# Kernel optimization log

Measured on AMD Instinct MI355X. Metric: run time of the kernel, lower is better.

Reference implementation:

```python
import jax, jax.numpy as jnp
import numpy as np

B, T, D, H, K = 2, 2048, 1024, 16, 4
DH = D // H  # 64 head dim
EPS_L2 = 1e-6
EPS_RMS = 1e-6


def setup_inputs() -> dict:
    key = jax.random.key(0)
    ks = jax.random.split(key, 10)
    s = 0.02
    return {
        'x': jax.random.normal(ks[0], (B, T, D), jnp.float32),
        'Wq': jax.random.normal(ks[1], (D, D), jnp.float32) * s,
        'Wk': jax.random.normal(ks[2], (D, D), jnp.float32) * s,
        'Wv': jax.random.normal(ks[3], (D, D), jnp.float32) * s,
        'Wb': jax.random.normal(ks[4], (D, H), jnp.float32) * s,
        'conv_q': jax.random.normal(ks[5], (D, K), jnp.float32) * 0.5,
        'conv_k': jax.random.normal(ks[6], (D, K), jnp.float32) * 0.5,
        'conv_v': jax.random.normal(ks[7], (D, K), jnp.float32) * 0.5,
        'rms_g': jnp.ones((DH,), jnp.float32),
        'Wo': jax.random.normal(ks[8], (D, D), jnp.float32) * s,
    }


def _silu(u):
    return u * jax.nn.sigmoid(u)


def _short_conv(x, w):
    # causal depthwise conv1d, x: [B,T,C], w: [C,K]; y[t] = sum_i w[:,i]*x[t-(K-1)+i]
    k = w.shape[1]
    xp = jnp.pad(x, ((0, 0), (k - 1, 0), (0, 0)))
    y = xp[:, 0:T, :] * w[:, 0]
    for i in range(1, k):
        y = y + xp[:, i:i + T, :] * w[:, i]
    return y


def _l2norm(u):
    return u * jax.lax.rsqrt(jnp.sum(u * u, axis=-1, keepdims=True) + EPS_L2)


def reference(x, Wq, Wk, Wv, Wb, conv_q, conv_k, conv_v, rms_g, Wo):
    # projections + causal short conv (silu fused, as in fla ShortConvolution)
    q = _silu(_short_conv(x @ Wq, conv_q)).reshape(B, T, H, DH)
    k = _silu(_short_conv(x @ Wk, conv_k)).reshape(B, T, H, DH)
    v = _silu(_short_conv(x @ Wv, conv_v)).reshape(B, T, H, DH)
    q = _l2norm(q)
    k = _l2norm(k)
    beta = jax.nn.sigmoid(x @ Wb)  # [B,T,H]

    # time-major for scan
    qs = q.transpose(1, 0, 2, 3)  # [T,B,H,DH]
    ks_ = k.transpose(1, 0, 2, 3)
    vs = v.transpose(1, 0, 2, 3)
    bs = beta.transpose(1, 0, 2)  # [T,B,H]

    def step(S, inp):
        # S: [B,H,dk,dv]; delta rule: S <- S + beta * k (v - k^T S)^T
        q_t, k_t, v_t, b_t = inp
        kS = jnp.einsum('bhk,bhkv->bhv', k_t, S)
        S = S + jnp.einsum('bhk,bhv->bhkv', k_t, b_t[..., None] * (v_t - kS))
        o_t = jnp.einsum('bhk,bhkv->bhv', q_t, S)
        return S, o_t

    S0 = jnp.zeros((B, H, DH, DH), x.dtype)
    _, o = jax.lax.scan(step, S0, (qs, ks_, vs, bs))  # o: [T,B,H,DH]
    o = o.transpose(1, 0, 2, 3)  # [B,T,H,DH]

    # per-head RMSNorm then output projection
    o = o * jax.lax.rsqrt(jnp.mean(o * o, axis=-1, keepdims=True) + EPS_RMS) * rms_g
    return o.reshape(B, T, D) @ Wo
```

## Files before the change

kernel.cpp:

```cpp
#include <hip/hip_runtime.h>
#include <hip/hip_bf16.h>
#include <math.h>

#define B_ 2
#define T_ 2048
#define D_ 1024
#define H_ 16
#define DH_ 64
#define M_ (B_*T_)
#define NC_ 32
#define CS_ 64
#define NCH_ (B_*H_*NC_)
#define QKVN_ 3072

typedef __attribute__((ext_vector_type(4))) float floatx4;
typedef __attribute__((ext_vector_type(8))) short short8;

__device__ __forceinline__ ushort f2bf(float f) {
  union { float f; unsigned u; } c; c.f = f;
  unsigned r = (c.u + 0x7FFFu + ((c.u >> 16) & 1u)) >> 16;
  return (ushort)r;
}
__device__ __forceinline__ float siluf(float u) {
  return u / (1.f + __expf(-u));
}
__device__ __forceinline__ float f4get(const float4& v, int j) {
  return j == 0 ? v.x : j == 1 ? v.y : j == 2 ? v.z : v.w;
}
__device__ __forceinline__ float rdlane(float v, int l) {
  return __int_as_float(__builtin_amdgcn_readlane(__float_as_int(v), l));
}
__device__ __forceinline__ int ksw(int r, int c) { return ((c ^ (r >> 4)) << 2); }

__global__ void cast_kernel(const float* __restrict__ in, ushort* __restrict__ out, int n4) {
  int i = blockIdx.x * blockDim.x + threadIdx.x;
  if (i >= n4) return;
  float4 v = ((const float4*)in)[i];
  ushort4 o;
  o.x = f2bf(v.x); o.y = f2bf(v.y); o.z = f2bf(v.z); o.w = f2bf(v.w);
  ((ushort4*)out)[i] = o;
}

__global__ void transpose_cast_kernel(const float* __restrict__ W, ushort* __restrict__ Wt,
                                      int K, int N) {
  __shared__ float tile[32][33];
  int tx = threadIdx.x, ty = threadIdx.y;
  int n0 = blockIdx.x * 32, k0 = blockIdx.y * 32;
  #pragma unroll
  for (int i = 0; i < 32; i += 8)
    tile[ty + i][tx] = W[(size_t)(k0 + ty + i) * N + n0 + tx];
  __syncthreads();
  #pragma unroll
  for (int i = 0; i < 32; i += 8)
    Wt[(size_t)(n0 + ty + i) * K + k0 + tx] = f2bf(tile[tx][ty + i]);
}

__global__ void transpose_wb_kernel(const float* __restrict__ Wb, float* __restrict__ WbT) {
  int bk = blockIdx.x;
  int tid = threadIdx.x;
  int kl = tid >> 4, h = tid & 15;
  int k = bk * 16 + kl;
  WbT[(size_t)h * D_ + k] = Wb[(size_t)k * H_ + h];
}

__global__ __launch_bounds__(256) void gemm128_kernel(
    const ushort* __restrict__ A, const ushort* __restrict__ Bt,
    float* __restrict__ C, int M, int N, int K) {
  __shared__ ushort lA[128 * 32];
  __shared__ ushort lB[128 * 32];
  int tid = threadIdx.x;
  int wave = tid >> 6, lane = tid & 63;
  int wm = wave >> 1, wn = wave & 1;
  int m16 = lane & 15, q4 = lane >> 4;
  int bm = blockIdx.x, bn = blockIdx.y;
  floatx4 acc[4][4] = {};
  int srow = tid >> 2;
  int sk8 = tid & 3;
  const ushort* Ag = A + (size_t)(bm * 128 + srow) * K + sk8 * 8;
  const ushort* Bg = Bt + (size_t)(bn * 128 + srow) * K + sk8 * 8;
  ushort* lAp = lA + tid * 8;
  ushort* lBp = lB + tid * 8;
  for (int k0 = 0; k0 < K; k0 += 32) {
    __builtin_amdgcn_global_load_lds(
        (const __attribute__((address_space(1))) void*)(Ag + k0),
        (__attribute__((address_space(3))) void*)lAp, 16, 0, 0);
    __builtin_amdgcn_global_load_lds(
        (const __attribute__((address_space(1))) void*)(Ag + (size_t)64 * K + k0),
        (__attribute__((address_space(3))) void*)(lAp + 2048), 16, 0, 0);
    __builtin_amdgcn_global_load_lds(
        (const __attribute__((address_space(1))) void*)(Bg + k0),
        (__attribute__((address_space(3))) void*)lBp, 16, 0, 0);
    __builtin_amdgcn_global_load_lds(
        (const __attribute__((address_space(1))) void*)(Bg + (size_t)64 * K + k0),
        (__attribute__((address_space(3))) void*)(lBp + 2048), 16, 0, 0);
    __syncthreads();
    short8 af[4], bf[4];
    #pragma unroll
    for (int i = 0; i < 4; i++) {
      af[i] = *(short8*)&lA[(wm * 64 + i * 16 + m16) * 32 + q4 * 8];
      bf[i] = *(short8*)&lB[(wn * 64 + i * 16 + m16) * 32 + q4 * 8];
    }
    #pragma unroll
    for (int mi = 0; mi < 4; mi++)
      #pragma unroll
      for (int nj = 0; nj < 4; nj++)
        acc[mi][nj] = __builtin_amdgcn_mfma_f32_16x16x32_bf16(af[mi], bf[nj], acc[mi][nj], 0, 0, 0);
    __syncthreads();
  }
  float* Cb = C + (size_t)(bm * 128) * N + bn * 128;
  #pragma unroll
  for (int mi = 0; mi < 4; mi++) {
    #pragma unroll
    for (int nj = 0; nj < 4; nj++) {
      #pragma unroll
      for (int i = 0; i < 4; i++) {
        int row = wm * 64 + mi * 16 + q4 * 4 + i;
        int col = wn * 64 + nj * 16 + m16;
        Cb[(size_t)row * N + col] = acc[mi][nj][i];
      }
    }
  }
}

__global__ __launch_bounds__(256) void beta_kernel(const float* __restrict__ x,
                                                   const float* __restrict__ WbT,
                                                   float* __restrict__ beta) {
  __shared__ __align__(16) float xs[D_];
  int row = blockIdx.x;
  int tid = threadIdx.x;
  ((float4*)xs)[tid] = ((const float4*)(x + (size_t)row * D_))[tid];
  __syncthreads();
  int h = tid >> 4;
  int seg = tid & 15;
  const float4* wrow = (const float4*)(WbT + (size_t)h * D_) + seg * 16;
  const float4* xsrow = (const float4*)xs + seg * 16;
  float s = 0.f;
  #pragma unroll
  for (int j = 0; j < 16; j++) {
    int jj = (j + seg) & 15;
    float4 xv = xsrow[jj];
    float4 wv = wrow[jj];
    s += xv.x * wv.x + xv.y * wv.y + xv.z * wv.z + xv.w * wv.w;
  }
  #pragma unroll
  for (int off = 8; off; off >>= 1) s += __shfl_down(s, off, 16);
  if (seg == 0) beta[(size_t)row * H_ + h] = 1.f / (1.f + __expf(-s));
}

__global__ __launch_bounds__(256) void conv_kernel(
    const float* __restrict__ qkv,
    const float* __restrict__ cq, const float* __restrict__ ck, const float* __restrict__ cv,
    float* __restrict__ qo, float* __restrict__ ko, float* __restrict__ vo) {
  int row = blockIdx.x;
  int t = row & (T_ - 1);
  int tid = threadIdx.x;
  int c0 = tid * 4;
  float4 zf = {0.f, 0.f, 0.f, 0.f};
  float4 xq[4], xk[4], xv[4];
  #pragma unroll
  for (int i = 0; i < 4; i++) {
    int tt = t - 3 + i;
    if (tt >= 0) {
      const float* rp = qkv + (size_t)(row - 3 + i) * QKVN_;
      xq[i] = *(const float4*)(rp + c0);
      xk[i] = *(const float4*)(rp + 1024 + c0);
      xv[i] = *(const float4*)(rp + 2048 + c0);
    } else { xq[i] = zf; xk[i] = zf; xv[i] = zf; }
  }
  float yq[4], yk[4], yv[4];
  float pq = 0.f, pk = 0.f;
  #pragma unroll
  for (int j = 0; j < 4; j++) {
    float4 wq = ((const float4*)cq)[c0 + j];
    float4 wk = ((const float4*)ck)[c0 + j];
    float4 wv = ((const float4*)cv)[c0 + j];
    float sq = 0.f, sk = 0.f, sv = 0.f;
    #pragma unroll
    for (int i = 0; i < 4; i++) {
      sq += f4get(wq, i) * f4get(xq[i], j);
      sk += f4get(wk, i) * f4get(xk[i], j);
      sv += f4get(wv, i) * f4get(xv[i], j);
    }
    yq[j] = siluf(sq); yk[j] = siluf(sk); yv[j] = siluf(sv);
    pq += yq[j] * yq[j]; pk += yk[j] * yk[j];
  }
  #pragma unroll
  for (int off = 1; off < 16; off <<= 1) {
    pq += __shfl_xor(pq, off, 16);
    pk += __shfl_xor(pk, off, 16);
  }
  float rq = rsqrtf(pq + 1e-6f), rk = rsqrtf(pk + 1e-6f);
  float4 oq = {yq[0]*rq, yq[1]*rq, yq[2]*rq, yq[3]*rq};
  float4 okk = {yk[0]*rk, yk[1]*rk, yk[2]*rk, yk[3]*rk};
  float4 ov = {yv[0], yv[1], yv[2], yv[3]};
  *(float4*)(qo + (size_t)row * D_ + c0) = oq;
  *(float4*)(ko + (size_t)row * D_ + c0) = okk;
  *(float4*)(vo + (size_t)row * D_ + c0) = ov;
}

__global__ __launch_bounds__(256) void prep1_kernel(
    const float* __restrict__ kn, const float* __restrict__ vn,
    const float* __restrict__ beta,
    float* __restrict__ Wkbuf, float* __restrict__ U0buf) {
  __shared__ __align__(16) float Ash[64 * 68];
  __shared__ float bsh[64];
  __shared__ __align__(16) float uni[5312];
  float (*Ksh)[68] = (float (*)[68])uni;
  float (*Tsh)[16][20] = (float (*)[16][20])uni;
  float (*Msh)[16][20] = (float (*)[16][20])(uni + 1280);
  float (*Xsh)[132] = (float (*)[132])(uni + 3200);

  int ch = blockIdx.x;
  int b = ch >> 9, h = (ch >> 5) & 15, c = ch & 31;
  int tid = threadIdx.x;
  int t = tid >> 2, seg = tid & 3;
  int wave = tid >> 6, lane = tid & 63;
  int r = lane >> 2, q = lane & 3;
  const float* krow = kn + ((size_t)(b * T_ + c * 64 + t)) * D_ + h * 64;
  #pragma unroll
  for (int g = 0; g < 4; g++)
    *(float4*)&Ksh[t][ksw(t, seg * 4 + g)] = *(const float4*)&krow[seg * 16 + 4 * g];
  if (tid < 64) bsh[tid] = beta[((size_t)(b * T_ + c * 64 + tid)) * H_ + h];
  __syncthreads();
  {
    int qt = tid >> 4, qs = tid & 15;
    int swt = qt >> 2, sws = qs >> 2;
    float acc[4][4];
    #pragma unroll
    for (int i = 0; i < 4; i++)
      #pragma unroll
      for (int j = 0; j < 4; j++) acc[i][j] = 0.f;
    for (int d4 = 0; d4 < 16; d4++) {
      float4 kt[4], ks[4];
      #pragma unroll
      for (int i = 0; i < 4; i++) kt[i] = *(float4*)&Ksh[qt * 4 + i][((d4 ^ swt) << 2)];
      #pragma unroll
      for (int j = 0; j < 4; j++) ks[j] = *(float4*)&Ksh[qs * 4 + j][((d4 ^ sws) << 2)];
      #pragma unroll
      for (int i = 0; i < 4; i++)
        #pragma unroll
        for (int j = 0; j < 4; j++)
          acc[i][j] += kt[i].x * ks[j].x + kt[i].y * ks[j].y
                     + kt[i].z * ks[j].z + kt[i].w * ks[j].w;
    }
    #pragma unroll
    for (int i = 0; i < 4; i++) {
      int row = qt * 4 + i;
      float bt = bsh[row];
      float4 a4;
      a4.x = (row > qs * 4 + 0) ? bt * acc[i][0] : 0.f;
      a4.y = (row > qs * 4 + 1) ? bt * acc[i][1] : 0.f;
      a4.z = (row > qs * 4 + 2) ? bt * acc[i][2] : 0.f;
      a4.w = (row > qs * 4 + 3) ? bt * acc[i][3] : 0.f;
      *(float4*)&Ash[row * 68 + qs * 4] = a4;
    }
  }
  float xk[16], xv[16];
  {
    float bt = bsh[t];
    const float* vrow = vn + ((size_t)(b * T_ + c * 64 + t)) * D_ + h * 64;
    #pragma unroll
    for (int g = 0; g < 4; g++) {
      float4 kv = *(float4*)&Ksh[t][ksw(t, seg * 4 + g)];
      float4 vv = *(const float4*)&vrow[seg * 16 + 4 * g];
      xk[4*g+0] = bt * kv.x; xk[4*g+1] = bt * kv.y; xk[4*g+2] = bt * kv.z; xk[4*g+3] = bt * kv.w;
      xv[4*g+0] = bt * vv.x; xv[4*g+1] = bt * vv.y; xv[4*g+2] = bt * vv.z; xv[4*g+3] = bt * vv.w;
    }
  }
  __syncthreads();
  {
    float a[16];
    #pragma unroll
    for (int i = 0; i < 16; i++) a[i] = Ash[(wave * 16 + r) * 68 + wave * 16 + i];
    float4 w4 = {0.f, 0.f, 0.f, 0.f};
    if ((r >> 2) == q) ((float*)&w4)[r & 3] = 1.f;
    #pragma unroll
    for (int i = 0; i < 15; i++) {
      int src = i * 4 + q;
      float4 wi;
      wi.x = __shfl(w4.x, src, 64);
      wi.y = __shfl(w4.y, src, 64);
      wi.z = __shfl(w4.z, src, 64);
      wi.w = __shfl(w4.w, src, 64);
      if (r > i) {
        w4.x -= a[i] * wi.x; w4.y -= a[i] * wi.y;
        w4.z -= a[i] * wi.z; w4.w -= a[i] * wi.w;
      }
    }
    *(float4*)&Tsh[wave][r][q * 4] = w4;
  }
  __syncthreads();
  for (int k = 0; k < wave; k++) {
    float4 m4 = {0.f, 0.f, 0.f, 0.f};
    #pragma unroll
    for (int i = 0; i < 16; i++) {
      float aik = Ash[(wave * 16 + r) * 68 + k * 16 + i];
      float4 tk = *(float4*)&Tsh[k][i][q * 4];
      m4.x += aik * tk.x; m4.y += aik * tk.y;
      m4.z += aik * tk.z; m4.w += aik * tk.w;
    }
    int mi = wave * (wave - 1) / 2 + k;
    *(float4*)&Msh[mi][r][q * 4] = m4;
  }
  float* wkout = &Wkbuf[(size_t)ch * 4096 + t * 64];
  float* u0out = &U0buf[(size_t)ch * 4096 + t * 64];
  for (int k = 0; k < 4; k++) {
    if (wave == k) {
      #pragma unroll
      for (int g = 0; g < 4; g++) {
        float4 k4 = {xk[4*g+0], xk[4*g+1], xk[4*g+2], xk[4*g+3]};
        float4 v4 = {xv[4*g+0], xv[4*g+1], xv[4*g+2], xv[4*g+3]};
        *(float4*)&Xsh[r][seg * 16 + 4 * g] = k4;
        *(float4*)&Xsh[r][64 + seg * 16 + 4 * g] = v4;
      }
    }
    __syncthreads();
    if (wave == k) {
      float nk[16], nv[16];
      #pragma unroll
      for (int i2 = 0; i2 < 16; i2++) { nk[i2] = 0.f; nv[i2] = 0.f; }
      #pragma unroll
      for (int i = 0; i < 16; i++) {
        float tc = Tsh[k][r][i];
        #pragma unroll
        for (int g = 0; g < 4; g++) {
          float4 yk = *(float4*)&Xsh[i][seg * 16 + 4 * g];
          float4 yv = *(float4*)&Xsh[i][64 + seg * 16 + 4 * g];
          nk[4*g+0] += tc * yk.x; nk[4*g+1] += tc * yk.y;
          nk[4*g+2] += tc * yk.z; nk[4*g+3] += tc * yk.w;
          nv[4*g+0] += tc * yv.x; nv[4*g+1] += tc * yv.y;
          nv[4*g+2] += tc * yv.z; nv[4*g+3] += tc * yv.w;
        }
      }
      #pragma unroll
      for (int g = 0; g < 4; g++) {
        float4 k4 = {nk[4*g+0], nk[4*g+1], nk[4*g+2], nk[4*g+3]};
        float4 v4 = {nv[4*g+0], nv[4*g+1], nv[4*g+2], nv[4*g+3]};
        *(float4*)&wkout[seg * 16 + 4 * g] = k4;
        *(float4*)&u0out[seg * 16 + 4 * g] = v4;
      }
    } else if (wave > k) {
      int mi = wave * (wave - 1) / 2 + k;
      #pragma unroll
      for (int i = 0; i < 16; i++) {
        float mc = Msh[mi][r][i];
        #pragma unroll
        for (int g = 0; g < 4; g++) {
          float4 yk = *(float4*)&Xsh[i][seg * 16 + 4 * g];
          float4 yv = *(float4*)&Xsh[i][64 + seg * 16 + 4 * g];
          xk[4*g+0] -= mc * yk.x; xk[4*g+1] -= mc * yk.y;
          xk[4*g+2] -= mc * yk.z; xk[4*g+3] -= mc * yk.w;
          xv[4*g+0] -= mc * yv.x; xv[4*g+1] -= mc * yv.y;
          xv[4*g+2] -= mc * yv.z; xv[4*g+3] -= mc * yv.w;
        }
      }
    }
    __syncthreads();
  }
}

__global__ __launch_bounds__(256) void prep2ab_kernel(
    float* qn, const float* __restrict__ kn,
    const float* __restrict__ Wkbuf, const float* __restrict__ U0buf,
    float* __restrict__ O0buf) {
  __shared__ float Qsh[64][68];
  __shared__ float Ksh[64][68];
  __shared__ float Lsh[64][68];
  float (*Wksh)[68] = Qsh;
  float (*U0sh)[68] = Ksh;
  int ch = blockIdx.x;
  int b = ch >> 9, h = (ch >> 5) & 15, c = ch & 31;
  int tid = threadIdx.x;
  int t = tid >> 2, seg = tid & 3;
  const float* qrow = qn + ((size_t)(b * T_ + c * 64 + t)) * D_ + h * 64;
  const float* krow = kn + ((size_t)(b * T_ + c * 64 + t)) * D_ + h * 64;
  #pragma unroll
  for (int g = 0; g < 4; g++) {
    *(float4*)&Qsh[t][seg * 16 + 4 * g] = *(const float4*)&qrow[seg * 16 + 4 * g];
    *(float4*)&Ksh[t][ksw(t, seg * 4 + g)] = *(const float4*)&krow[seg * 16 + 4 * g];
  }
  __syncthreads();
  {
    int qt = tid >> 4, qs = tid & 15;
    int sws = qs >> 2;
    float acc[4][4];
    #pragma unroll
    for (int i = 0; i < 4; i++)
      #pragma unroll
      for (int j = 0; j < 4; j++) acc[i][j] = 0.f;
    for (int d4 = 0; d4 < 16; d4++) {
      float4 qv[4], ks[4];
      #pragma unroll
      for (int i = 0; i < 4; i++) qv[i] = *(float4*)&Qsh[qt * 4 + i][d4 * 4];
      #pragma unroll
      for (int j = 0; j < 4; j++) ks[j] = *(float4*)&Ksh[qs * 4 + j][((d4 ^ sws) << 2)];
      #pragma unroll
      for (int i = 0; i < 4; i++)
        #pragma unroll
        for (int j = 0; j < 4; j++)
          acc[i][j] += qv[i].x * ks[j].x + qv[i].y * ks[j].y
                     + qv[i].z * ks[j].z + qv[i].w * ks[j].w;
    }
    #pragma unroll
    for (int i = 0; i < 4; i++) {
      int row = qt * 4 + i;
      float4 ov;
      ov.x = (qs * 4 + 0 <= row) ? acc[i][0] : 0.f;
      ov.y = (qs * 4 + 1 <= row) ? acc[i][1] : 0.f;
      ov.z = (qs * 4 + 2 <= row) ? acc[i][2] : 0.f;
      ov.w = (qs * 4 + 3 <= row) ? acc[i][3] : 0.f;
      *(float4*)&Lsh[row][qs * 4] = ov;
    }
  }
  __syncthreads();
  #pragma unroll
  for (int g = 0; g < 4; g++) {
    int o = t * 64 + seg * 16 + 4 * g;
    *(float4*)&Wksh[t][seg * 16 + 4 * g] = *(const float4*)&Wkbuf[(size_t)ch * 4096 + o];
    *(float4*)&U0sh[t][seg * 16 + 4 * g] = *(const float4*)&U0buf[(size_t)ch * 4096 + o];
  }
  __syncthreads();
  int j0 = seg * 16;
  float o0[16], lw[16];
  #pragma unroll
  for (int r = 0; r < 16; r++) { o0[r] = 0.f; lw[r] = 0.f; }
  for (int s = 0; s <= t; s++) {
    float l = Lsh[t][s];
    #pragma unroll
    for (int g = 0; g < 4; g++) {
      float4 u = *(float4*)&U0sh[s][j0 + 4 * g];
      float4 w = *(float4*)&Wksh[s][j0 + 4 * g];
      o0[4*g+0] += l * u.x; o0[4*g+1] += l * u.y; o0[4*g+2] += l * u.z; o0[4*g+3] += l * u.w;
      lw[4*g+0] += l * w.x; lw[4*g+1] += l * w.y; lw[4*g+2] += l * w.z; lw[4*g+3] += l * w.w;
    }
  }
  float* qwrow = qn + ((size_t)(b * T_ + c * 64 + t)) * D_ + h * 64;
  #pragma unroll
  for (int g = 0; g < 4; g++) {
    float4 qv = *(const float4*)&qwrow[j0 + 4 * g];
    qv.x -= lw[4*g+0]; qv.y -= lw[4*g+1]; qv.z -= lw[4*g+2]; qv.w -= lw[4*g+3];
    *(float4*)&qwrow[j0 + 4 * g] = qv;
    float4 ov = {o0[4*g+0], o0[4*g+1], o0[4*g+2], o0[4*g+3]};
    *(float4*)&O0buf[(size_t)ch * 4096 + t * 64 + j0 + 4 * g] = ov;
  }
}

__global__ __launch_bounds__(256) void prep2c_kernel(
    float* kn, const float* __restrict__ Wkbuf,
    const float* __restrict__ U0buf, float* __restrict__ Pbuf) {
  __shared__ float Ksh[64][68];
  __shared__ float Wksh[64][68];
  __shared__ float U0sh[64][68];
  int ch = blockIdx.x;
  int b = ch >> 9, h = (ch >> 5) & 15, c = ch & 31;
  int tid = threadIdx.x;
  int t = tid >> 2, seg = tid & 3;
  const float* krow = kn + ((size_t)(b * T_ + c * 64 + t)) * D_ + h * 64;
  #pragma unroll
  for (int g = 0; g < 4; g++) {
    int o = t * 64 + seg * 16 + 4 * g;
    *(float4*)&Ksh[t][seg * 16 + 4 * g]  = *(const float4*)&krow[seg * 16 + 4 * g];
    *(float4*)&Wksh[t][seg * 16 + 4 * g] = *(const float4*)&Wkbuf[(size_t)ch * 4096 + o];
    *(float4*)&U0sh[t][seg * 16 + 4 * g] = *(const float4*)&U0buf[(size_t)ch * 4096 + o];
  }
  __syncthreads();
  int d0 = seg * 16;
  float accP[16], accZ[16];
  #pragma unroll
  for (int r = 0; r < 16; r++) { accP[r] = 0.f; accZ[r] = 0.f; }
  for (int s = 0; s < 64; s++) {
    float kt = Ksh[s][t];
    float u  = U0sh[s][t];
    #pragma unroll
    for (int g = 0; g < 4; g++) {
      float4 w4 = *(float4*)&Wksh[s][d0 + 4 * g];
      float4 k4 = *(float4*)&Ksh[s][d0 + 4 * g];
      accP[4*g+0] += kt * w4.x; accP[4*g+1] += kt * w4.y; accP[4*g+2] += kt * w4.z; accP[4*g+3] += kt * w4.w;
      accZ[4*g+0] += u * k4.x;  accZ[4*g+1] += u * k4.y;  accZ[4*g+2] += u * k4.z;  accZ[4*g+3] += u * k4.w;
    }
  }
  float* zrow = kn + ((size_t)(b * T_ + c * 64 + t)) * D_ + h * 64;
  #pragma unroll
  for (int g = 0; g < 4; g++) {
    float4 pv;
    pv.x = ((d0 + 4*g + 0) == t ? 1.f : 0.f) - accP[4*g+0];
    pv.y = ((d0 + 4*g + 1) == t ? 1.f : 0.f) - accP[4*g+1];
    pv.z = ((d0 + 4*g + 2) == t ? 1.f : 0.f) - accP[4*g+2];
    pv.w = ((d0 + 4*g + 3) == t ? 1.f : 0.f) - accP[4*g+3];
    *(float4*)&Pbuf[(size_t)ch * 4096 + (size_t)(seg * 4 + g) * 256 + (size_t)t * 4] = pv;
    float4 zv = {accZ[4*g+0], accZ[4*g+1], accZ[4*g+2], accZ[4*g+3]};
    *(float4*)&zrow[d0 + 4 * g] = zv;
  }
}

__global__ __launch_bounds__(256) void state_kernel(
    const float* __restrict__ kn , const float* __restrict__ Pbuf ,
    float* __restrict__ Sbuf) {
  __shared__ __align__(16) float Pl[2][4096];
  int bid = blockIdx.x;
  int bh = bid & 31, js = bid >> 5;
  int h = bh & 15, b = bh >> 4;
  int tid = threadIdx.x;
  int wv = tid >> 6, lane = tid & 63;
  int j0 = js * 4 + wv;
  float s0 = 0.f;
  const size_t bhNC = (size_t)bh * NC_;
  const float* Pg0 = Pbuf + bhNC * 4096;
  #pragma unroll
  for (int g = 0; g < 4; g++)
    __builtin_amdgcn_global_load_lds(
        (const __attribute__((address_space(1))) void*)(Pg0 + (g * 256 + tid) * 4),
        (__attribute__((address_space(3))) void*)&Pl[0][(g * 256 + tid) * 4], 16, 0, 0);
  float zn = kn[((size_t)(b * T_ + j0)) * D_ + h * 64 + lane];
  int cur = 0;
  #pragma unroll 1
  for (int c = 0; c < NC_; c++) {
    __syncthreads();
    float z = zn;
    size_t ch = bhNC + c;
    if (c + 1 < NC_) {
      const float* Pg = Pbuf + (ch + 1) * 4096;
      #pragma unroll
      for (int g = 0; g < 4; g++)
        __builtin_amdgcn_global_load_lds(
            (const __attribute__((address_space(1))) void*)(Pg + (g * 256 + tid) * 4),
            (__attribute__((address_space(3))) void*)&Pl[cur ^ 1][(g * 256 + tid) * 4], 16, 0, 0);
      zn = kn[((size_t)(b * T_ + (c + 1) * 64 + j0)) * D_ + h * 64 + lane];
    }
    Sbuf[ch * 4096 + (size_t)j0 * 64 + lane] = s0;
    float acc = z;
    #pragma unroll
    for (int f = 0; f < 16; f++) {
      floatx4 pv = *(floatx4*)&Pl[cur][f * 256 + lane * 4];
      acc += pv.x * rdlane(s0, f * 4 + 0);
      acc += pv.y * rdlane(s0, f * 4 + 1);
      acc += pv.z * rdlane(s0, f * 4 + 2);
      acc += pv.w * rdlane(s0, f * 4 + 3);
    }
    s0 = acc;
    cur ^= 1;
  }
}

__global__ __launch_bounds__(256) void ophase_kernel(
    const float* __restrict__ qn , const float* __restrict__ Sbuf,
    const float* __restrict__ O0buf, const float* __restrict__ rms_g,
    ushort* __restrict__ ob) {
  __shared__ float Ssht[64][68];
  __shared__ float QshT[64][65];
  __shared__ float part[64][4];
  int ch = blockIdx.x;
  int b = ch >> 9, h = (ch >> 5) & 15, c = ch & 31;
  int tid = threadIdx.x;
  int t = tid & 63, jg = tid >> 6;
  #pragma unroll
  for (int g = 0; g < 4; g++) {
    int idx = tid + g * 256;
    *(float4*)&Ssht[idx >> 4][(idx & 15) * 4] =
        *(const float4*)&Sbuf[(size_t)ch * 4096 + (size_t)idx * 4];
  }
  #pragma unroll
  for (int g = 0; g < 4; g++) {
    int idx = tid + g * 256;
    int row = idx >> 4, c4 = idx & 15;
    float4 qv = *(const float4*)&qn[((size_t)(b * T_ + c * 64 + row)) * D_ + h * 64 + c4 * 4];
    QshT[c4 * 4 + 0][row] = qv.x;
    QshT[c4 * 4 + 1][row] = qv.y;
    QshT[c4 * 4 + 2][row] = qv.z;
    QshT[c4 * 4 + 3][row] = qv.w;
  }
  float o[16];
  #pragma unroll
  for (int g = 0; g < 4; g++) {
    float4 o4 = *(const float4*)&O0buf[(size_t)ch * 4096 + t * 64 + jg * 16 + g * 4];
    o[4*g+0] = o4.x; o[4*g+1] = o4.y; o[4*g+2] = o4.z; o[4*g+3] = o4.w;
  }
  __syncthreads();
  for (int d4 = 0; d4 < 16; d4++) {
    float q0 = QshT[d4 * 4 + 0][t];
    float q1 = QshT[d4 * 4 + 1][t];
    float q2 = QshT[d4 * 4 + 2][t];
    float q3 = QshT[d4 * 4 + 3][t];
    #pragma unroll
    for (int r = 0; r < 16; r++) {
      float4 s4 = *(float4*)&Ssht[jg * 16 + r][d4 * 4];
      o[r] += q0 * s4.x + q1 * s4.y + q2 * s4.z + q3 * s4.w;
    }
  }
  float ss = 0.f;
  #pragma unroll
  for (int r = 0; r < 16; r++) ss += o[r] * o[r];
  part[t][jg] = ss;
  __syncthreads();
  float tot = part[t][0] + part[t][1] + part[t][2] + part[t][3];
  float sc = rsqrtf(tot * (1.f / 64.f) + 1e-6f);
  ushort* orow = &ob[((size_t)(b * T_ + c * 64 + t)) * D_ + h * 64];
  #pragma unroll
  for (int g = 0; g < 4; g++) {
    float4 g4 = *(const float4*)&rms_g[jg * 16 + g * 4];
    ushort4 r4;
    r4.x = f2bf(o[4*g+0] * sc * g4.x); r4.y = f2bf(o[4*g+1] * sc * g4.y);
    r4.z = f2bf(o[4*g+2] * sc * g4.z); r4.w = f2bf(o[4*g+3] * sc * g4.w);
    *(ushort4*)&orow[jg * 16 + g * 4] = r4;
  }
}

extern "C" void kernel_launch(void* const* d_in, const int* in_sizes, int n_in,
                              void* d_out, int out_size, void* d_ws, size_t ws_size,
                              hipStream_t stream) {
  const float* x  = (const float*)d_in[0];
  const float* Wq = (const float*)d_in[1];
  const float* Wk = (const float*)d_in[2];
  const float* Wv = (const float*)d_in[3];
  const float* Wb = (const float*)d_in[4];
  const float* cq = (const float*)d_in[5];
  const float* ck = (const float*)d_in[6];
  const float* cv = (const float*)d_in[7];
  const float* rg = (const float*)d_in[8];
  const float* Wo = (const float*)d_in[9];
  float* out = (float*)d_out;
  char* ws = (char*)d_ws;
  const size_t MiB = 1ull << 20;
  ushort* xb   = (ushort*)(ws + 0);
  ushort* Wqt  = (ushort*)(ws + 8 * MiB);
  ushort* Wkt  = (ushort*)(ws + 10 * MiB);
  ushort* Wvt  = (ushort*)(ws + 12 * MiB);
  ushort* Wot  = (ushort*)(ws + 14 * MiB);
  float* qkv   = (float*)(ws + 16 * MiB);
  float* qn    = (float*)(ws + 64 * MiB);
  float* kn    = (float*)(ws + 80 * MiB);
  float* vn    = (float*)(ws + 96 * MiB);
  float* beta  = (float*)(ws + 112 * MiB);
  float* WbT   = (float*)(ws + 112 * MiB + 256 * 1024);
  float* Wkbuf = (float*)(ws + 16 * MiB);
  float* U0buf = (float*)(ws + 32 * MiB);
  float* Pbuf  = (float*)(ws + 48 * MiB);
  float* O0buf = (float*)(ws + 96 * MiB);
  float* Sbuf  = (float*)(ws + 16 * MiB);
  ushort* ob   = (ushort*)(ws + 0);

  hipLaunchKernelGGL(cast_kernel, dim3(M_ * D_ / 4 / 256), dim3(256), 0, stream,
                     x, xb, M_ * D_ / 4);
  dim3 tb(32, 8);
  hipLaunchKernelGGL(transpose_cast_kernel, dim3(32, 32), tb, 0, stream, Wq, Wqt, D_, D_);
  hipLaunchKernelGGL(transpose_cast_kernel, dim3(32, 32), tb, 0, stream, Wk, Wkt, D_, D_);
  hipLaunchKernelGGL(transpose_cast_kernel, dim3(32, 32), tb, 0, stream, Wv, Wvt, D_, D_);
  hipLaunchKernelGGL(transpose_cast_kernel, dim3(32, 32), tb, 0, stream, Wo, Wot, D_, D_);
  hipLaunchKernelGGL(transpose_wb_kernel, dim3(64), dim3(256), 0, stream, Wb, WbT);

  hipLaunchKernelGGL(gemm128_kernel, dim3(M_ / 128, QKVN_ / 128), dim3(256), 0, stream,
                     xb, Wqt, qkv, M_, QKVN_, D_);

  hipLaunchKernelGGL(beta_kernel, dim3(M_), dim3(256), 0, stream, x, WbT, beta);
  hipLaunchKernelGGL(conv_kernel, dim3(M_), dim3(256), 0, stream,
                     qkv, cq, ck, cv, qn, kn, vn);

  hipLaunchKernelGGL(prep1_kernel, dim3(NCH_), dim3(256), 0, stream,
                     kn, vn, beta, Wkbuf, U0buf);
  hipLaunchKernelGGL(prep2ab_kernel, dim3(NCH_), dim3(256), 0, stream,
                     qn, kn, Wkbuf, U0buf, O0buf);
  hipLaunchKernelGGL(prep2c_kernel, dim3(NCH_), dim3(256), 0, stream,
                     kn, Wkbuf, U0buf, Pbuf);
  hipLaunchKernelGGL(state_kernel, dim3(512), dim3(256), 0, stream,
                     kn, Pbuf, Sbuf);
  hipLaunchKernelGGL(ophase_kernel, dim3(NCH_), dim3(256), 0, stream,
                     qn, Sbuf, O0buf, rg, ob);
  hipLaunchKernelGGL(gemm128_kernel, dim3(M_ / 128, D_ / 128), dim3(256), 0, stream,
                     ob, Wot, out, M_, D_, D_);
}
```

Before: 396.7 us.

## Double-buffer LDS in bf16 GEMM and swizzle block order for L2 reuse

Adds a second LDS buffer so global-to-LDS loads for the next K step are issued before computing on the current one. Explicit vmcnt waits and raw barriers replace __syncthreads. Block indices are remapped through an XCD-aware swizzle into 8x8 supertiles to improve cache locality. It doubles LDS use and assumes grid dimensions divisible by 8 and supertile counts that fit the remap.

```diff
diff --git a/kernel.cpp b/kernel.cpp
--- a/kernel.cpp
+++ b/kernel.cpp
@@ -66,47 +66,71 @@
 __global__ __launch_bounds__(256) void gemm128_kernel(
     const ushort* __restrict__ A, const ushort* __restrict__ Bt,
     float* __restrict__ C, int M, int N, int K) {
-  __shared__ ushort lA[128 * 32];
-  __shared__ ushort lB[128 * 32];
+  __shared__ ushort lA[2][128 * 32];
+  __shared__ ushort lB[2][128 * 32];
   int tid = threadIdx.x;
   int wave = tid >> 6, lane = tid & 63;
   int wm = wave >> 1, wn = wave & 1;
   int m16 = lane & 15, q4 = lane >> 4;
-  int bm = blockIdx.x, bn = blockIdx.y;
+  int nbm = gridDim.x, nbn = gridDim.y;
+  int lin = blockIdx.y * nbm + blockIdx.x;
+  int cpx = (nbm * nbn) >> 3;
+  int swz = (lin & 7) * cpx + (lin >> 3);
+  int stn = nbn >> 3;
+  int st = swz >> 6, in_ = swz & 63;
+  int stm = st / stn, soff = st - stm * stn;
+  int bm = stm * 8 + (in_ & 7);
+  int bn = soff * 8 + (in_ >> 3);
   floatx4 acc[4][4] = {};
   int srow = tid >> 2;
   int sk8 = tid & 3;
   const ushort* Ag = A + (size_t)(bm * 128 + srow) * K + sk8 * 8;
   const ushort* Bg = Bt + (size_t)(bn * 128 + srow) * K + sk8 * 8;
-  ushort* lAp = lA + tid * 8;
-  ushort* lBp = lB + tid * 8;
-  for (int k0 = 0; k0 < K; k0 += 32) {
-    __builtin_amdgcn_global_load_lds(
-        (const __attribute__((address_space(1))) void*)(Ag + k0),
-        (__attribute__((address_space(3))) void*)lAp, 16, 0, 0);
-    __builtin_amdgcn_global_load_lds(
-        (const __attribute__((address_space(1))) void*)(Ag + (size_t)64 * K + k0),
-        (__attribute__((address_space(3))) void*)(lAp + 2048), 16, 0, 0);
-    __builtin_amdgcn_global_load_lds(
-        (const __attribute__((address_space(1))) void*)(Bg + k0),
-        (__attribute__((address_space(3))) void*)lBp, 16, 0, 0);
-    __builtin_amdgcn_global_load_lds(
-        (const __attribute__((address_space(1))) void*)(Bg + (size_t)64 * K + k0),
-        (__attribute__((address_space(3))) void*)(lBp + 2048), 16, 0, 0);
-    __syncthreads();
+  int nks = K >> 5;
+
+#define GSTAGE(bufi, kk0)                                                       \
+  {                                                                             \
+    __builtin_amdgcn_global_load_lds(                                           \
+        (const __attribute__((address_space(1))) void*)(Ag + (kk0)),            \
+        (__attribute__((address_space(3))) void*)&lA[bufi][tid * 8], 16, 0, 0); \
+    __builtin_amdgcn_global_load_lds(                                           \
+        (const __attribute__((address_space(1))) void*)(Ag + (size_t)64 * K + (kk0)), \
+        (__attribute__((address_space(3))) void*)&lA[bufi][tid * 8 + 2048], 16, 0, 0); \
+    __builtin_amdgcn_global_load_lds(                                           \
+        (const __attribute__((address_space(1))) void*)(Bg + (kk0)),            \
+        (__attribute__((address_space(3))) void*)&lB[bufi][tid * 8], 16, 0, 0); \
+    __builtin_amdgcn_global_load_lds(                                           \
+        (const __attribute__((address_space(1))) void*)(Bg + (size_t)64 * K + (kk0)), \
+        (__attribute__((address_space(3))) void*)&lB[bufi][tid * 8 + 2048], 16, 0, 0); \
+  }
+
+  GSTAGE(0, 0);
+  int cur = 0;
+  #pragma unroll 1
+  for (int ks = 0; ks < nks; ++ks) {
+    if (ks + 1 < nks) {
+      GSTAGE(cur ^ 1, (ks + 1) * 32);
+      asm volatile("s_waitcnt vmcnt(4)" ::: "memory");
+    } else {
+      asm volatile("s_waitcnt vmcnt(0)" ::: "memory");
+    }
+    __builtin_amdgcn_s_barrier();
+    __builtin_amdgcn_sched_barrier(0);
     short8 af[4], bf[4];
     #pragma unroll
     for (int i = 0; i < 4; i++) {
-      af[i] = *(short8*)&lA[(wm * 64 + i * 16 + m16) * 32 + q4 * 8];
-      bf[i] = *(short8*)&lB[(wn * 64 + i * 16 + m16) * 32 + q4 * 8];
+      af[i] = *(short8*)&lA[cur][(wm * 64 + i * 16 + m16) * 32 + q4 * 8];
+      bf[i] = *(short8*)&lB[cur][(wn * 64 + i * 16 + m16) * 32 + q4 * 8];
     }
     #pragma unroll
     for (int mi = 0; mi < 4; mi++)
       #pragma unroll
       for (int nj = 0; nj < 4; nj++)
         acc[mi][nj] = __builtin_amdgcn_mfma_f32_16x16x32_bf16(af[mi], bf[nj], acc[mi][nj], 0, 0, 0);
-    __syncthreads();
-  }
+    __builtin_amdgcn_s_barrier();
+    cur ^= 1;
+  }
+#undef GSTAGE
   float* Cb = C + (size_t)(bm * 128) * N + bn * 128;
   #pragma unroll
   for (int mi = 0; mi < 4; mi++) {
```

Result: faster. 378.7 us (-4.5%).
